# Kernel optimization log

Measured on AMD Instinct MI355X. Metric: run time of the kernel, lower is better.

The kernel has to match this reference:

```python
import jax, jax.numpy as jnp
import numpy as np

VOCAB = 32000
EMB = 512
HID = 512
MAX_LEN = 32
SOS = 1
PAD = 0


def setup_inputs() -> dict:
    key = jax.random.key(0)
    ks = jax.random.split(key, 9)
    s = 1.0 / np.sqrt(HID)
    emb = jax.random.normal(ks[0], (VOCAB, EMB), jnp.float32)
    emb = emb.at[PAD].set(0.0)  # padding_idx row is zeros
    return {
        "encoder_hidden": jax.random.normal(ks[1], (1, 64, HID), jnp.float32),
        "encoder_c": jax.random.normal(ks[2], (1, 64, HID), jnp.float32),
        "emb": emb,
        "W_ih": jax.random.uniform(ks[3], (4 * HID, EMB), jnp.float32, -s, s),
        "W_hh": jax.random.uniform(ks[4], (4 * HID, HID), jnp.float32, -s, s),
        "b_ih": jax.random.uniform(ks[5], (4 * HID,), jnp.float32, -s, s),
        "b_hh": jax.random.uniform(ks[6], (4 * HID,), jnp.float32, -s, s),
        "fc_w": jax.random.uniform(ks[7], (VOCAB, HID), jnp.float32, -s, s),
        "fc_b": jax.random.uniform(ks[8], (VOCAB,), jnp.float32, -s, s),
    }


def reference(encoder_hidden, encoder_c, emb, W_ih, W_hh, b_ih, b_hh, fc_w, fc_b):
    B = encoder_hidden.shape[1]
    h0 = encoder_hidden[0]  # [B,H] (num_layers == 1)
    c0 = encoder_c[0]
    tok0 = jnp.full((B,), SOS, jnp.int32)
    bias = b_ih + b_hh  # [4H]

    def step(carry, _):
        tok, h, c = carry
        x = emb[tok]  # [B,E] embedding gather
        gates = x @ W_ih.T + h @ W_hh.T + bias  # [B,4H]
        i, f, g, o = jnp.split(gates, 4, axis=-1)  # torch gate order i,f,g,o
        c = jax.nn.sigmoid(f) * c + jax.nn.sigmoid(i) * jnp.tanh(g)
        h = jax.nn.sigmoid(o) * jnp.tanh(c)
        logp = jax.nn.log_softmax(h @ fc_w.T + fc_b, axis=-1)  # [B,V]
        tok_next = jnp.argmax(logp, axis=-1).astype(jnp.int32)  # greedy topk(k=1)
        return (tok_next, h, c), logp

    (_, hT, _), logps = jax.lax.scan(step, (tok0, h0, c0), None, length=MAX_LEN + 1)
    decoder_outputs = jnp.transpose(logps, (1, 0, 2))  # [B, T, V]
    decoder_hidden = hT[None]  # [1, B, H]
    return decoder_outputs, decoder_hidden
```

## Files before the change

kernel.cpp:

```cpp
#include <hip/hip_runtime.h>
#include <math.h>

#define VOCABN 32000
#define HIDN 512
#define BN 64
#define TSTEPS 33
#define OUTROWS (TSTEPS * VOCABN)
#define NVBLK 500
#define NVT 2000
#define GSLICE 8

typedef float f4 __attribute__((ext_vector_type(4)));
typedef __bf16 bf16x8 __attribute__((ext_vector_type(8)));
typedef unsigned short u16x8 __attribute__((ext_vector_type(8)));

__device__ __forceinline__ unsigned short f2bf_rn(float f) {
    unsigned int u = __builtin_bit_cast(unsigned int, f);
    u += 0x7FFFu + ((u >> 16) & 1u);
    return (unsigned short)(u >> 16);
}
__device__ __forceinline__ float bfbits2f(unsigned short s) {
    unsigned int u = ((unsigned int)s) << 16;
    return __builtin_bit_cast(float, u);
}
__device__ __forceinline__ float sigf(float x) { return 1.f / (1.f + expf(-x)); }
__device__ __forceinline__ void olmerge(float& m, float& s, int& idx,
                                        float mo, float so, int io) {
    float M = fmaxf(m, mo);
    s = s * __expf(m - M) + so * __expf(mo - M);
    idx = (mo > m) ? io : ((mo == m) ? (io < idx ? io : idx) : idx);
    m = M;
}

__global__ __launch_bounds__(256) void k_init(const float* __restrict__ eh,
                                              const float* __restrict__ ec,
                                              float* __restrict__ h,
                                              float* __restrict__ c,
                                              int* __restrict__ tok) {
    int i = blockIdx.x * 256 + threadIdx.x;
    if (i < BN * HIDN) { h[i] = eh[i]; c[i] = ec[i]; }
    if (i < BN) tok[i] = 1;
}

__global__ __launch_bounds__(256) void k_conv(const float* __restrict__ fc_w,
                                              unsigned short* __restrict__ whiP,
                                              unsigned short* __restrict__ wloP) {
    const int vt = blockIdx.x;
    const int tid = threadIdx.x;
    #pragma unroll
    for (int i = 0; i < 4; ++i) {
        const int s = tid + 256 * i;
        const int kc = s >> 6, lane = s & 63;
        const int v = vt * 16 + (lane & 15);
        const int k = kc * 32 + (lane >> 4) * 8;
        const float* src = fc_w + (size_t)v * 512 + k;
        f4 a = *(const f4*)src;
        f4 b = *(const f4*)(src + 4);
        u16x8 hi, lo;
        #pragma unroll
        for (int e = 0; e < 4; ++e) {
            unsigned short ha = f2bf_rn(a[e]);
            hi[e] = ha; lo[e] = f2bf_rn(a[e] - bfbits2f(ha));
            unsigned short hb = f2bf_rn(b[e]);
            hi[4 + e] = hb; lo[4 + e] = f2bf_rn(b[e] - bfbits2f(hb));
        }
        const size_t o = ((size_t)(vt * 16 + kc) * 64 + lane) * 8;
        *(u16x8*)&whiP[o] = hi;
        *(u16x8*)&wloP[o] = lo;
    }
}

__global__ __launch_bounds__(256) void k_gates(const float* __restrict__ W_ih,
                                               const float* __restrict__ W_hh,
                                               const float* __restrict__ emb,
                                               const float* __restrict__ h,
                                               const int* __restrict__ tok,
                                               float* __restrict__ part) {
    __shared__ float w_s[64][68];
    __shared__ float x_s[64][68];
    const int tid = threadIdx.x;
    const int j0 = (blockIdx.x & 31) * 64;
    const int ks = blockIdx.x >> 5;
    const int k0 = ks * 128;
    const int tx = tid & 15;
    const int ty = tid >> 4;
    const int r  = tid >> 2;
    const int cq = (tid & 3) * 16;

    float acc[4][4];
    #pragma unroll
    for (int i = 0; i < 4; ++i)
        #pragma unroll
        for (int j = 0; j < 4; ++j) acc[i][j] = 0.f;

    for (int kk = 0; kk < 128; kk += 64) {
        const int k = k0 + kk;
        __syncthreads();
        {
            const float* src = (k < 512) ? (W_ih + (size_t)(j0 + r) * 512 + k + cq)
                                         : (W_hh + (size_t)(j0 + r) * 512 + (k - 512) + cq);
            const f4* s4 = (const f4*)src;
            f4* d4 = (f4*)&w_s[r][cq];
            d4[0] = s4[0]; d4[1] = s4[1]; d4[2] = s4[2]; d4[3] = s4[3];
        }
        {
            const float* src = (k < 512) ? (emb + (size_t)tok[r] * 512 + k + cq)
                                         : (h + (size_t)r * 512 + (k - 512) + cq);
            const f4* s4 = (const f4*)src;
            f4* d4 = (f4*)&x_s[r][cq];
            d4[0] = s4[0]; d4[1] = s4[1]; d4[2] = s4[2]; d4[3] = s4[3];
        }
        __syncthreads();
        #pragma unroll 4
        for (int c4 = 0; c4 < 64; c4 += 4) {
            f4 wv[4], xv[4];
            #pragma unroll
            for (int jj = 0; jj < 4; ++jj) wv[jj] = *(const f4*)&w_s[16 * jj + tx][c4];
            #pragma unroll
            for (int bb = 0; bb < 4; ++bb) xv[bb] = *(const f4*)&x_s[16 * bb + ty][c4];
            #pragma unroll
            for (int e = 0; e < 4; ++e)
                #pragma unroll
                for (int bb = 0; bb < 4; ++bb)
                    #pragma unroll
                    for (int jj = 0; jj < 4; ++jj)
                        acc[bb][jj] += xv[bb][e] * wv[jj][e];
        }
    }
    #pragma unroll
    for (int bb = 0; bb < 4; ++bb) {
        const int b = 16 * bb + ty;
        #pragma unroll
        for (int jj = 0; jj < 4; ++jj)
            part[((size_t)(ks * 64 + b)) * 2048 + j0 + 16 * jj + tx] = acc[bb][jj];
    }
}

__global__ __launch_bounds__(256) void k_cell(const float* __restrict__ part,
                                              const float* __restrict__ b_ih,
                                              const float* __restrict__ b_hh,
                                              float* __restrict__ h,
                                              float* __restrict__ c,
                                              unsigned short* __restrict__ hhi,
                                              unsigned short* __restrict__ hlo) {
    const int e = blockIdx.x * 256 + threadIdx.x;
    const int b = e >> 9, u = e & 511;
    float g[4];
    #pragma unroll
    for (int gi = 0; gi < 4; ++gi) {
        const int j = gi * 512 + u;
        float s = b_ih[j] + b_hh[j];
        #pragma unroll
        for (int ks = 0; ks < GSLICE; ++ks) s += part[((size_t)(ks * 64 + b)) * 2048 + j];
        g[gi] = s;
    }
    const float ig = sigf(g[0]);
    const float fg = sigf(g[1]);
    const float gg = tanhf(g[2]);
    const float og = sigf(g[3]);
    const float cn = fg * c[e] + ig * gg;
    const float hn = og * tanhf(cn);
    c[e] = cn;
    h[e] = hn;
    const unsigned short hi = f2bf_rn(hn);
    hhi[e] = hi;
    hlo[e] = f2bf_rn(hn - bfbits2f(hi));
}

__global__ __launch_bounds__(256) void k_logits(const unsigned short* __restrict__ whiP,
                                                const unsigned short* __restrict__ wloP,
                                                const float* __restrict__ fc_b,
                                                const unsigned short* __restrict__ hhi,
                                                const unsigned short* __restrict__ hlo,
                                                float* __restrict__ outrow,
                                                float* __restrict__ pm,
                                                float* __restrict__ ps,
                                                int* __restrict__ pi) {
    __shared__ float red_m[4 * 64];
    __shared__ float red_s[4 * 64];
    __shared__ int   red_i[4 * 64];

    const int tid  = threadIdx.x;
    const int w    = tid >> 6;
    const int lane = tid & 63;
    const int li   = lane & 15;
    const int lg   = lane >> 4;
    const int vt   = blockIdx.x * 4 + w;

    f4 acc[4];
    #pragma unroll
    for (int bf = 0; bf < 4; ++bf) acc[bf] = (f4){0.f, 0.f, 0.f, 0.f};

    const unsigned short* Ah = whiP + (size_t)vt * 8192 + lane * 8;
    const unsigned short* Al = wloP + (size_t)vt * 8192 + lane * 8;
    int boff[4];
    #pragma unroll
    for (int bf = 0; bf < 4; ++bf) boff[bf] = (li + 16 * bf) * 512 + lg * 8;

    #pragma unroll 4
    for (int kc = 0; kc < 16; ++kc) {
        bf16x8 Avh = *(const bf16x8*)(Ah + kc * 512);
        bf16x8 Avl = *(const bf16x8*)(Al + kc * 512);
        #pragma unroll
        for (int bf = 0; bf < 4; ++bf) {
            bf16x8 Bh = *(const bf16x8*)&hhi[boff[bf] + kc * 32];
            bf16x8 Bl = *(const bf16x8*)&hlo[boff[bf] + kc * 32];
            acc[bf] = __builtin_amdgcn_mfma_f32_16x16x32_bf16(Avh, Bh, acc[bf], 0, 0, 0);
            acc[bf] = __builtin_amdgcn_mfma_f32_16x16x32_bf16(Avl, Bh, acc[bf], 0, 0, 0);
            acc[bf] = __builtin_amdgcn_mfma_f32_16x16x32_bf16(Avh, Bl, acc[bf], 0, 0, 0);
        }
    }

    const int vbase = vt * 16;
    const f4 bias = *(const f4*)&fc_b[vbase + lg * 4];

    #pragma unroll
    for (int bf = 0; bf < 4; ++bf) {
        f4 x = acc[bf] + bias;
        acc[bf] = x;
        const int b = li + 16 * bf;
        *(f4*)&outrow[(size_t)b * OUTROWS + vbase + lg * 4] = x;
    }

    #pragma unroll
    for (int bf = 0; bf < 4; ++bf) {
        float m = -1e30f; int idx = 0;
        #pragma unroll
        for (int rg = 0; rg < 4; ++rg) {
            float x = acc[bf][rg];
            if (x > m) { m = x; idx = vbase + lg * 4 + rg; }
        }
        float s = 0.f;
        #pragma unroll
        for (int rg = 0; rg < 4; ++rg) s += __expf(acc[bf][rg] - m);
        #pragma unroll
        for (int off = 16; off <= 32; off <<= 1) {
            float mo = __shfl_xor(m, off);
            float so = __shfl_xor(s, off);
            int   io = __shfl_xor(idx, off);
            olmerge(m, s, idx, mo, so, io);
        }
        if (lg == 0) {
            red_m[w * 64 + li + 16 * bf] = m;
            red_s[w * 64 + li + 16 * bf] = s;
            red_i[w * 64 + li + 16 * bf] = idx;
        }
    }
    __syncthreads();
    if (tid < 64) {
        float m = red_m[tid]; float s = red_s[tid]; int idx = red_i[tid];
        #pragma unroll
        for (int w2 = 1; w2 < 4; ++w2)
            olmerge(m, s, idx, red_m[w2 * 64 + tid], red_s[w2 * 64 + tid], red_i[w2 * 64 + tid]);
        pm[blockIdx.x * 64 + tid] = m;
        ps[blockIdx.x * 64 + tid] = s;
        pi[blockIdx.x * 64 + tid] = idx;
    }
}

__global__ __launch_bounds__(256) void k_combine(const float* __restrict__ pm,
                                                 const float* __restrict__ ps,
                                                 const int* __restrict__ pi,
                                                 int* __restrict__ tok,
                                                 float* __restrict__ Lb, int t) {
    __shared__ float sm[256], ss[256];
    __shared__ int si[256];
    const int b = blockIdx.x;
    const int tid = threadIdx.x;
    float m = -1e30f, s = 0.f; int idx = 0;
    for (int blk = tid; blk < NVBLK; blk += 256)
        olmerge(m, s, idx, pm[blk * 64 + b], ps[blk * 64 + b], pi[blk * 64 + b]);
    sm[tid] = m; ss[tid] = s; si[tid] = idx;
    __syncthreads();
    for (int st = 128; st; st >>= 1) {
        if (tid < st) {
            float m0 = sm[tid], s0 = ss[tid]; int i0 = si[tid];
            olmerge(m0, s0, i0, sm[tid + st], ss[tid + st], si[tid + st]);
            sm[tid] = m0; ss[tid] = s0; si[tid] = i0;
        }
        __syncthreads();
    }
    if (tid == 0) { tok[b] = si[0]; Lb[t * 64 + b] = sm[0] + logf(ss[0]); }
}

__global__ __launch_bounds__(256) void k_sub(float* __restrict__ out,
                                             const float* __restrict__ Lb) {
    const int N4 = BN * OUTROWS / 4;
    for (int i4 = blockIdx.x * 256 + threadIdx.x; i4 < N4; i4 += gridDim.x * 256) {
        const int i = i4 * 4;
        const int b = i / OUTROWS;
        const int rem = i - b * OUTROWS;
        const int t = rem / VOCABN;
        f4 x = *(const f4*)&out[i];
        const float L = Lb[t * 64 + b];
        x[0] -= L; x[1] -= L; x[2] -= L; x[3] -= L;
        *(f4*)&out[i] = x;
    }
}

__global__ __launch_bounds__(256) void k_copyh(const float* __restrict__ h,
                                               float* __restrict__ dst) {
    int i = blockIdx.x * 256 + threadIdx.x;
    if (i < BN * HIDN) dst[i] = h[i];
}

__global__ __launch_bounds__(256) void k_logits_f32(const float* __restrict__ fc_w,
                                                    const float* __restrict__ fc_b,
                                                    const float* __restrict__ h,
                                                    float* __restrict__ outrow) {
    __shared__ float w_s[64][68];
    __shared__ float h_s[64][68];
    const int tid = threadIdx.x;
    const int v0 = blockIdx.x * 64;
    const int tx = tid & 15;
    const int ty = tid >> 4;
    const int r  = tid >> 2;
    const int cq = (tid & 3) * 16;

    float acc[4][4];
    #pragma unroll
    for (int i = 0; i < 4; ++i)
        #pragma unroll
        for (int j = 0; j < 4; ++j) acc[i][j] = 0.f;

    for (int k = 0; k < 512; k += 64) {
        __syncthreads();
        {
            const f4* s4 = (const f4*)(fc_w + (size_t)(v0 + r) * 512 + k + cq);
            f4* d4 = (f4*)&w_s[r][cq];
            d4[0] = s4[0]; d4[1] = s4[1]; d4[2] = s4[2]; d4[3] = s4[3];
        }
        {
            const f4* s4 = (const f4*)(h + (size_t)r * 512 + k + cq);
            f4* d4 = (f4*)&h_s[r][cq];
            d4[0] = s4[0]; d4[1] = s4[1]; d4[2] = s4[2]; d4[3] = s4[3];
        }
        __syncthreads();
        #pragma unroll 4
        for (int c4 = 0; c4 < 64; c4 += 4) {
            f4 wv[4], hv[4];
            #pragma unroll
            for (int vv = 0; vv < 4; ++vv) wv[vv] = *(const f4*)&w_s[16 * vv + tx][c4];
            #pragma unroll
            for (int bb = 0; bb < 4; ++bb) hv[bb] = *(const f4*)&h_s[16 * bb + ty][c4];
            #pragma unroll
            for (int e = 0; e < 4; ++e)
                #pragma unroll
                for (int bb = 0; bb < 4; ++bb)
                    #pragma unroll
                    for (int vv = 0; vv < 4; ++vv)
                        acc[bb][vv] += hv[bb][e] * wv[vv][e];
        }
    }
    float bias[4];
    #pragma unroll
    for (int vv = 0; vv < 4; ++vv) bias[vv] = fc_b[v0 + 16 * vv + tx];
    #pragma unroll
    for (int bb = 0; bb < 4; ++bb) {
        const int b = 16 * bb + ty;
        #pragma unroll
        for (int vv = 0; vv < 4; ++vv)
            outrow[(size_t)b * OUTROWS + v0 + 16 * vv + tx] = acc[bb][vv] + bias[vv];
    }
}

__global__ __launch_bounds__(1024) void k_softmax(float* __restrict__ outrow,
                                                  int* __restrict__ tok) {
    const int b = blockIdx.x, tid = threadIdx.x;
    float* row = outrow + (size_t)b * OUTROWS;
    __shared__ float sm[1024];
    __shared__ int si[1024];

    float m = -1e30f; int mi = 0;
    for (int v = tid; v < VOCABN; v += 1024) {
        float x = row[v];
        if (x > m) { m = x; mi = v; }
    }
    sm[tid] = m; si[tid] = mi;
    __syncthreads();
    for (int s = 512; s; s >>= 1) {
        if (tid < s) {
            float xo = sm[tid + s]; int io = si[tid + s];
            if (xo > sm[tid] || (xo == sm[tid] && io < si[tid])) { sm[tid] = xo; si[tid] = io; }
        }
        __syncthreads();
    }
    const float M = sm[0];
    const int ami = si[0];
    __syncthreads();

    float sum = 0.f;
    for (int v = tid; v < VOCABN; v += 1024) sum += __expf(row[v] - M);
    sm[tid] = sum;
    __syncthreads();
    for (int s = 512; s; s >>= 1) {
        if (tid < s) sm[tid] += sm[tid + s];
        __syncthreads();
    }
    const float L = M + logf(sm[0]);
    if (tid == 0) tok[b] = ami;

    for (int v = tid; v < VOCABN; v += 1024) row[v] = row[v] - L;
}

extern "C" void kernel_launch(void* const* d_in, const int* in_sizes, int n_in,
                              void* d_out, int out_size, void* d_ws, size_t ws_size,
                              hipStream_t stream) {
    const float* enc_h = (const float*)d_in[0];
    const float* enc_c = (const float*)d_in[1];
    const float* emb   = (const float*)d_in[2];
    const float* W_ih  = (const float*)d_in[3];
    const float* W_hh  = (const float*)d_in[4];
    const float* b_ih  = (const float*)d_in[5];
    const float* b_hh  = (const float*)d_in[6];
    const float* fc_w  = (const float*)d_in[7];
    const float* fc_b  = (const float*)d_in[8];
    float* out = (float*)d_out;

    char* cur = (char*)d_ws;
    float* h    = (float*)cur;            cur += 32768 * 4;
    float* c    = (float*)cur;            cur += 32768 * 4;
    float* part = (float*)cur;            cur += (size_t)GSLICE * 64 * 2048 * 4;
    unsigned short* hhi = (unsigned short*)cur; cur += 32768 * 2;
    unsigned short* hlo = (unsigned short*)cur; cur += 32768 * 2;
    float* pm   = (float*)cur;            cur += (size_t)NVBLK * 64 * 4;
    float* ps   = (float*)cur;            cur += (size_t)NVBLK * 64 * 4;
    int*   pi   = (int*)cur;              cur += (size_t)NVBLK * 64 * 4;
    float* Lb   = (float*)cur;            cur += TSTEPS * 64 * 4;
    int*   tok  = (int*)cur;              cur += 64 * 4;
    unsigned short* whiP = (unsigned short*)cur; cur += (size_t)NVT * 8192 * 2;
    unsigned short* wloP = (unsigned short*)cur; cur += (size_t)NVT * 8192 * 2;
    const size_t NEED = (size_t)(cur - (char*)d_ws);

    if (ws_size >= NEED) {
        k_conv<<<NVT, 256, 0, stream>>>(fc_w, whiP, wloP);
        k_init<<<128, 256, 0, stream>>>(enc_h, enc_c, h, c, tok);
        for (int t = 0; t < TSTEPS; ++t) {
            k_gates<<<32 * GSLICE, 256, 0, stream>>>(W_ih, W_hh, emb, h, tok, part);
            k_cell<<<128, 256, 0, stream>>>(part, b_ih, b_hh, h, c, hhi, hlo);
            float* outrow = out + (size_t)t * VOCABN;
            k_logits<<<NVBLK, 256, 0, stream>>>(whiP, wloP, fc_b, hhi, hlo, outrow, pm, ps, pi);
            k_combine<<<64, 256, 0, stream>>>(pm, ps, pi, tok, Lb, t);
        }
        k_sub<<<2048, 256, 0, stream>>>(out, Lb);
        k_copyh<<<128, 256, 0, stream>>>(h, out + (size_t)BN * OUTROWS);
    } else {
        k_init<<<128, 256, 0, stream>>>(enc_h, enc_c, h, c, tok);
        for (int t = 0; t < TSTEPS; ++t) {
            k_gates<<<32 * GSLICE, 256, 0, stream>>>(W_ih, W_hh, emb, h, tok, part);
            k_cell<<<128, 256, 0, stream>>>(part, b_ih, b_hh, h, c, hhi, hlo);
            float* outrow = out + (size_t)t * VOCABN;
            k_logits_f32<<<500, 256, 0, stream>>>(fc_w, fc_b, h, outrow);
            k_softmax<<<64, 1024, 0, stream>>>(outrow, tok);
        }
        k_copyh<<<128, 256, 0, stream>>>(h, out + (size_t)BN * OUTROWS);
    }
}
```

Baseline: 1.949 ms.

## Split K across wave pairs in logits kernel, doubling block count

Each vocabulary tile in the logits GEMM is now computed by two waves, each handling half of the 512-wide hidden dimension. The partial accumulators are reduced through shared memory before the bias, output store and online softmax/argmax steps. Blocks now cover 2 tiles instead of 4, so the grid has twice as many blocks. The aim is more parallelism and shorter per-wave dependency chains, at the cost of an extra shared-memory reduction, a barrier, and idle waves during the epilogue.

```diff
diff --git a/kernel.cpp b/kernel.cpp
--- a/kernel.cpp
+++ b/kernel.cpp
@@ -6,7 +6,7 @@
 #define BN 64
 #define TSTEPS 33
 #define OUTROWS (TSTEPS * VOCABN)
-#define NVBLK 500
+#define NVBLK 1000
 #define NVT 2000
 #define GSLICE 8
 
@@ -167,38 +167,41 @@
     hlo[e] = f2bf_rn(hn - bfbits2f(hi));
 }
 
-__global__ __launch_bounds__(256) void k_logits(const unsigned short* __restrict__ whiP,
-                                                const unsigned short* __restrict__ wloP,
-                                                const float* __restrict__ fc_b,
-                                                const unsigned short* __restrict__ hhi,
-                                                const unsigned short* __restrict__ hlo,
-                                                float* __restrict__ outrow,
-                                                float* __restrict__ pm,
-                                                float* __restrict__ ps,
-                                                int* __restrict__ pi) {
-    __shared__ float red_m[4 * 64];
-    __shared__ float red_s[4 * 64];
-    __shared__ int   red_i[4 * 64];
+__global__ __launch_bounds__(256, 4) void k_logits(const unsigned short* __restrict__ whiP,
+                                                   const unsigned short* __restrict__ wloP,
+                                                   const float* __restrict__ fc_b,
+                                                   const unsigned short* __restrict__ hhi,
+                                                   const unsigned short* __restrict__ hlo,
+                                                   float* __restrict__ outrow,
+                                                   float* __restrict__ pm,
+                                                   float* __restrict__ ps,
+                                                   int* __restrict__ pi) {
+    __shared__ float sacc[2][16][64];
+    __shared__ float red_m[128];
+    __shared__ float red_s[128];
+    __shared__ int   red_i[128];
 
     const int tid  = threadIdx.x;
     const int w    = tid >> 6;
     const int lane = tid & 63;
     const int li   = lane & 15;
     const int lg   = lane >> 4;
-    const int vt   = blockIdx.x * 4 + w;
+    const int vtl  = w >> 1;
+    const int kh   = w & 1;
+    const int vt   = blockIdx.x * 2 + vtl;
 
     f4 acc[4];
     #pragma unroll
     for (int bf = 0; bf < 4; ++bf) acc[bf] = (f4){0.f, 0.f, 0.f, 0.f};
 
-    const unsigned short* Ah = whiP + (size_t)vt * 8192 + lane * 8;
-    const unsigned short* Al = wloP + (size_t)vt * 8192 + lane * 8;
+    const unsigned short* Ah = whiP + (size_t)vt * 8192 + kh * 4096 + lane * 8;
+    const unsigned short* Al = wloP + (size_t)vt * 8192 + kh * 4096 + lane * 8;
     int boff[4];
     #pragma unroll
-    for (int bf = 0; bf < 4; ++bf) boff[bf] = (li + 16 * bf) * 512 + lg * 8;
+    for (int bf = 0; bf < 4; ++bf) boff[bf] = (li + 16 * bf) * 512 + kh * 256 + lg * 8;
 
     #pragma unroll 4
-    for (int kc = 0; kc < 16; ++kc) {
+    for (int kc = 0; kc < 8; ++kc) {
         bf16x8 Avh = *(const bf16x8*)(Ah + kc * 512);
         bf16x8 Avl = *(const bf16x8*)(Al + kc * 512);
         #pragma unroll
@@ -211,47 +214,62 @@
         }
     }
 
-    const int vbase = vt * 16;
-    const f4 bias = *(const f4*)&fc_b[vbase + lg * 4];
-
-    #pragma unroll
-    for (int bf = 0; bf < 4; ++bf) {
-        f4 x = acc[bf] + bias;
-        acc[bf] = x;
-        const int b = li + 16 * bf;
-        *(f4*)&outrow[(size_t)b * OUTROWS + vbase + lg * 4] = x;
-    }
-
-    #pragma unroll
-    for (int bf = 0; bf < 4; ++bf) {
-        float m = -1e30f; int idx = 0;
-        #pragma unroll
-        for (int rg = 0; rg < 4; ++rg) {
-            float x = acc[bf][rg];
-            if (x > m) { m = x; idx = vbase + lg * 4 + rg; }
-        }
-        float s = 0.f;
-        #pragma unroll
-        for (int rg = 0; rg < 4; ++rg) s += __expf(acc[bf][rg] - m);
-        #pragma unroll
-        for (int off = 16; off <= 32; off <<= 1) {
-            float mo = __shfl_xor(m, off);
-            float so = __shfl_xor(s, off);
-            int   io = __shfl_xor(idx, off);
-            olmerge(m, s, idx, mo, so, io);
-        }
-        if (lg == 0) {
-            red_m[w * 64 + li + 16 * bf] = m;
-            red_s[w * 64 + li + 16 * bf] = s;
-            red_i[w * 64 + li + 16 * bf] = idx;
+    if (kh == 1) {
+        #pragma unroll
+        for (int bf = 0; bf < 4; ++bf)
+            #pragma unroll
+            for (int rg = 0; rg < 4; ++rg)
+                sacc[vtl][bf * 4 + rg][lane] = acc[bf][rg];
+    }
+    __syncthreads();
+
+    if (kh == 0) {
+        #pragma unroll
+        for (int bf = 0; bf < 4; ++bf)
+            #pragma unroll
+            for (int rg = 0; rg < 4; ++rg)
+                acc[bf][rg] += sacc[vtl][bf * 4 + rg][lane];
+
+        const int vbase = vt * 16;
+        const f4 bias = *(const f4*)&fc_b[vbase + lg * 4];
+
+        #pragma unroll
+        for (int bf = 0; bf < 4; ++bf) {
+            f4 x = acc[bf] + bias;
+            acc[bf] = x;
+            const int b = li + 16 * bf;
+            *(f4*)&outrow[(size_t)b * OUTROWS + vbase + lg * 4] = x;
+        }
+
+        #pragma unroll
+        for (int bf = 0; bf < 4; ++bf) {
+            float m = -1e30f; int idx = 0;
+            #pragma unroll
+            for (int rg = 0; rg < 4; ++rg) {
+                float x = acc[bf][rg];
+                if (x > m) { m = x; idx = vbase + lg * 4 + rg; }
+            }
+            float s = 0.f;
+            #pragma unroll
+            for (int rg = 0; rg < 4; ++rg) s += __expf(acc[bf][rg] - m);
+            #pragma unroll
+            for (int off = 16; off <= 32; off <<= 1) {
+                float mo = __shfl_xor(m, off);
+                float so = __shfl_xor(s, off);
+                int   io = __shfl_xor(idx, off);
+                olmerge(m, s, idx, mo, so, io);
+            }
+            if (lg == 0) {
+                red_m[vtl * 64 + li + 16 * bf] = m;
+                red_s[vtl * 64 + li + 16 * bf] = s;
+                red_i[vtl * 64 + li + 16 * bf] = idx;
+            }
         }
     }
     __syncthreads();
     if (tid < 64) {
         float m = red_m[tid]; float s = red_s[tid]; int idx = red_i[tid];
-        #pragma unroll
-        for (int w2 = 1; w2 < 4; ++w2)
-            olmerge(m, s, idx, red_m[w2 * 64 + tid], red_s[w2 * 64 + tid], red_i[w2 * 64 + tid]);
+        olmerge(m, s, idx, red_m[64 + tid], red_s[64 + tid], red_i[64 + tid]);
         pm[blockIdx.x * 64 + tid] = m;
         ps[blockIdx.x * 64 + tid] = s;
         pi[blockIdx.x * 64 + tid] = idx;
```

Result: no change. 1.943 ms, median of 2 (-0.3%).
